# Kernel optimization log

Hardware: AMD Instinct MI355X
Metric: run time of the kernel (lower is better)

## Reference

```python
import jax, jax.numpy as jnp
import numpy as np

STATE_DIM, FAST, SLOW, ACT, HID = 256, 32, 16, 4, 256
B, T = 256, 512


def _gelu(x):
    return jax.nn.gelu(x, approximate=False)


def _gru_cell(x, h, wih, whh, bih, bhh):
    # torch GRUCell: r,z,n gates; weights are [3H, in]/[3H, H]
    gi = x @ wih.T + bih
    gh = h @ whh.T + bhh
    ir, iz, inn = jnp.split(gi, 3, axis=-1)
    hr, hz, hn = jnp.split(gh, 3, axis=-1)
    r = jax.nn.sigmoid(ir + hr)
    z = jax.nn.sigmoid(iz + hz)
    n = jnp.tanh(inn + r * hn)
    return (1.0 - z) * n + z * h


def setup_inputs() -> dict:
    key = jax.random.key(0)
    ks = jax.random.split(key, 32)
    s = 0.05
    d = {
        'states': jax.random.normal(ks[0], (B, T, STATE_DIM), jnp.float32),
        'actions': jax.random.normal(ks[1], (B, T, ACT), jnp.float32),
        'noise_fast': jax.random.normal(ks[2], (B, T, FAST), jnp.float32),
        'noise_slow': jax.random.normal(ks[3], (B, T, SLOW), jnp.float32),
        # fast encoder: Linear(256,256) GELU Linear(256,64)
        'fe_w1': jax.random.normal(ks[4], (HID, STATE_DIM)) * s,
        'fe_b1': jnp.zeros((HID,)),
        'fe_w2': jax.random.normal(ks[5], (FAST * 2, HID)) * s,
        'fe_b2': jnp.zeros((FAST * 2,)),
        # fast GRUCell(in=36, h=32)
        'fg_wih': jax.random.normal(ks[6], (3 * FAST, FAST + ACT)) * s,
        'fg_whh': jax.random.normal(ks[7], (3 * FAST, FAST)) * s,
        'fg_bih': jnp.zeros((3 * FAST,)),
        'fg_bhh': jnp.zeros((3 * FAST,)),
        # slow encoder: Linear(288,128) GELU Linear(128,32)
        'se_w1': jax.random.normal(ks[8], (HID // 2, STATE_DIM + FAST)) * s,
        'se_b1': jnp.zeros((HID // 2,)),
        'se_w2': jax.random.normal(ks[9], (SLOW * 2, HID // 2)) * s,
        'se_b2': jnp.zeros((SLOW * 2,)),
        # slow GRUCell(in=48, h=16)
        'sg_wih': jax.random.normal(ks[10], (3 * SLOW, SLOW + FAST)) * s,
        'sg_whh': jax.random.normal(ks[11], (3 * SLOW, SLOW)) * s,
        'sg_bih': jnp.zeros((3 * SLOW,)),
        'sg_bhh': jnp.zeros((3 * SLOW,)),
        # decoder: Linear(48,256) GELU Linear(256,256)
        'de_w1': jax.random.normal(ks[12], (HID, FAST + SLOW)) * s,
        'de_b1': jnp.zeros((HID,)),
        'de_w2': jax.random.normal(ks[13], (STATE_DIM, HID)) * s,
        'de_b2': jnp.zeros((STATE_DIM,)),
        'slow_update_rate': jnp.asarray(0.1, jnp.float32),
    }
    return d


def _forward(states, actions, noise_fast, noise_slow,
             fe_w1, fe_b1, fe_w2, fe_b2, fg_wih, fg_whh, fg_bih, fg_bhh,
             se_w1, se_b1, se_w2, se_b2, sg_wih, sg_whh, sg_bih, sg_bhh,
             de_w1, de_b1, de_w2, de_b2, slow_update_rate):
    Bn = states.shape[0]
    upd = jax.nn.sigmoid(slow_update_rate)

    def step(carry, xs):
        z_fast, z_slow = carry
        state, action, nf, ns = xs  # [B, ...] per-timestep slices
        # fast encoder + reparameterization
        fp = _gelu(state @ fe_w1.T + fe_b1) @ fe_w2.T + fe_b2
        f_mean, f_lv = jnp.split(fp, 2, axis=-1)
        z_fast_new = f_mean + jnp.exp(0.5 * f_lv) * nf
        z_fast = _gru_cell(jnp.concatenate([z_fast_new, action], -1), z_fast,
                           fg_wih, fg_whh, fg_bih, fg_bhh)
        # slow encoder + reparameterization
        sp = _gelu(jnp.concatenate([state, z_fast], -1) @ se_w1.T + se_b1) @ se_w2.T + se_b2
        s_mean, s_lv = jnp.split(sp, 2, axis=-1)
        z_slow_new = s_mean + jnp.exp(0.5 * s_lv) * ns
        z_slow_trans = _gru_cell(jnp.concatenate([z_slow_new, z_fast], -1), z_slow,
                                 sg_wih, sg_whh, sg_bih, sg_bhh)
        z_slow = upd * z_slow_trans + (1.0 - upd) * z_slow
        # decoder
        pred = _gelu(jnp.concatenate([z_fast, z_slow], -1) @ de_w1.T + de_b1) @ de_w2.T + de_b2
        return (z_fast, z_slow), (z_fast, z_slow, pred)

    init = (jnp.zeros((Bn, FAST), states.dtype), jnp.zeros((Bn, SLOW), states.dtype))
    xs = (states.swapaxes(0, 1), actions.swapaxes(0, 1),
          noise_fast.swapaxes(0, 1), noise_slow.swapaxes(0, 1))  # time-major [T,B,*]
    _, (zf, zs, preds) = jax.lax.scan(step, init, xs)
    return (preds.swapaxes(0, 1), zf.swapaxes(0, 1), zs.swapaxes(0, 1))


def reference(states, actions, noise_fast, noise_slow,
              fe_w1, fe_b1, fe_w2, fe_b2, fg_wih, fg_whh, fg_bih, fg_bhh,
              se_w1, se_b1, se_w2, se_b2, sg_wih, sg_whh, sg_bih, sg_bhh,
              de_w1, de_b1, de_w2, de_b2, slow_update_rate):
    # returns (predictions [B,T,state_dim], fast_latents [B,T,32], slow_latents [B,T,16])
    return _forward(states, actions, noise_fast, noise_slow,
                    fe_w1, fe_b1, fe_w2, fe_b2, fg_wih, fg_whh, fg_bih, fg_bhh,
                    se_w1, se_b1, se_w2, se_b2, sg_wih, sg_whh, sg_bih, sg_bhh,
                    de_w1, de_b1, de_w2, de_b2, slow_update_rate)
```

## Files before the change

### kernel.cpp

```cpp
#include <hip/hip_runtime.h>

typedef unsigned short u16t;
typedef __attribute__((ext_vector_type(8))) short bf16x8;
typedef __attribute__((ext_vector_type(4))) float f32x4;
typedef __attribute__((ext_vector_type(2))) float f32x2;

#define DI static __device__ __forceinline__

constexpr int Bn = 256, Tn = 512;
constexpr long Rn = (long)Bn * Tn;

DI float b2f(u16t u){ union{unsigned u32; float f;} v; v.u32 = ((unsigned)u)<<16; return v.f; }
DI u16t f2b(float f){ union{float fp; unsigned u;} v; v.fp=f; return (u16t)((v.u + 0x7fffu + ((v.u>>16)&1u))>>16); }
DI float fsigm(float x){ return __builtin_amdgcn_rcpf(1.f + __expf(-x)); }
DI float ftanh(float x){ float e = __expf(2.f*x); return 1.f - 2.f*__builtin_amdgcn_rcpf(e+1.f); }
DI float fgelu(float x){
  float t = 0.7978845608028654f*x*(1.f + 0.044715f*x*x);
  return x*(1.f - __builtin_amdgcn_rcpf(__expf(2.f*t)+1.f));
}
DI f32x4 mfma16(bf16x8 a, bf16x8 b, f32x4 c){ return __builtin_amdgcn_mfma_f32_16x16x32_bf16(a,b,c,0,0,0); }
DI unsigned pkr(float a, float b){ return (unsigned)f2b(a) | ((unsigned)f2b(b)<<16); }
DI float plo(unsigned u){ union{unsigned x; float f;} v; v.x = u<<16; return v.f; }
DI float phi(unsigned u){ union{unsigned x; float f;} v; v.x = u & 0xffff0000u; return v.f; }
DI bf16x8 mk8(unsigned w0,unsigned w1,unsigned w2,unsigned w3){
  union{unsigned u[4]; bf16x8 v;} z; z.u[0]=w0; z.u[1]=w1; z.u[2]=w2; z.u[3]=w3; return z.v;
}
DI bf16x8 ldw8(const float* p){
  f32x4 a = *(const f32x4*)p, b = *(const f32x4*)(p+4);
  return mk8(pkr(a[0],a[1]), pkr(a[2],a[3]), pkr(b[0],b[1]), pkr(b[2],b[3]));
}
DI bf16x8 zero8(){ bf16x8 v; v[0]=0;v[1]=0;v[2]=0;v[3]=0;v[4]=0;v[5]=0;v[6]=0;v[7]=0; return v; }
DI void lfence(){ asm volatile("s_waitcnt lgkmcnt(0)" ::: "memory"); __builtin_amdgcn_sched_barrier(0); }

__global__ __launch_bounds__(256) void k_pre(
    const float* __restrict__ states, const float* __restrict__ nfast,
    const float* __restrict__ fe_w1, const float* __restrict__ fe_b1,
    const float* __restrict__ fe_w2, const float* __restrict__ fe_b2,
    const float* __restrict__ se_w1, const float* __restrict__ se_b1,
    u16t* __restrict__ ws_zfn, u16t* __restrict__ ws_se1)
{
  __shared__ __align__(16) u16t s_x[64*256];
  __shared__ __align__(16) u16t s_h[64*256];
  const int tid = threadIdx.x;
  const int lane = tid & 63, wave = tid >> 6;
  const int l15 = lane & 15, lh = lane >> 4;
  const long row0 = (long)blockIdx.x * 64;

  #pragma unroll
  for (int i=0;i<8;i++){
    int c = tid + i*256;
    int row = c >> 5, col = (c & 31) << 3;
    bf16x8 v = ldw8(states + (row0+row)*256 + col);
    *(bf16x8*)&s_x[row*256 + (col ^ ((row&7)<<3))] = v;
  }
  __syncthreads();

  const int wrow = wave*16;
  const int arow = wrow + l15;
  f32x4 acc1[16], acc3[8];
  #pragma unroll
  for (int nt=0;nt<16;nt++){ float bv = fe_b1[nt*16+l15]; acc1[nt] = (f32x4){bv,bv,bv,bv}; }
  #pragma unroll
  for (int nt=0;nt<8;nt++){ float bv = se_b1[nt*16+l15]; acc3[nt] = (f32x4){bv,bv,bv,bv}; }
  #pragma unroll
  for (int kt=0;kt<8;kt++){
    int acol = kt*32 + lh*8;
    bf16x8 af = *(const bf16x8*)&s_x[arow*256 + (acol ^ ((arow&7)<<3))];
    #pragma unroll
    for (int nt=0;nt<16;nt++){
      bf16x8 bw = ldw8(fe_w1 + (nt*16+l15)*256 + acol);
      acc1[nt] = mfma16(af, bw, acc1[nt]);
    }
    #pragma unroll
    for (int nt=0;nt<8;nt++){
      bf16x8 bw = ldw8(se_w1 + (nt*16+l15)*288 + acol);
      acc3[nt] = mfma16(af, bw, acc3[nt]);
    }
  }
  #pragma unroll
  for (int nt=0;nt<8;nt++){
    #pragma unroll
    for (int r=0;r<4;r++){
      int row = wrow + lh*4 + r;
      ws_se1[(row0+row)*128 + nt*16+l15] = f2b(acc3[nt][r]);
    }
  }
  #pragma unroll
  for (int nt=0;nt<16;nt++){
    #pragma unroll
    for (int r=0;r<4;r++){
      int row = wrow + lh*4 + r; int col = nt*16 + l15;
      s_h[row*256 + (col ^ ((row&7)<<3))] = f2b(fgelu(acc1[nt][r]));
    }
  }
  __syncthreads();
  f32x4 acc2[4];
  #pragma unroll
  for (int a=0;a<4;a++){ float bv = fe_b2[a*16+l15]; acc2[a] = (f32x4){bv,bv,bv,bv}; }
  #pragma unroll
  for (int kt=0;kt<8;kt++){
    int acol = kt*32 + lh*8;
    bf16x8 af = *(const bf16x8*)&s_h[arow*256 + (acol ^ ((arow&7)<<3))];
    #pragma unroll
    for (int a=0;a<4;a++){
      bf16x8 bw = ldw8(fe_w2 + (a*16+l15)*256 + acol);
      acc2[a] = mfma16(af, bw, acc2[a]);
    }
  }
  #pragma unroll
  for (int a=0;a<2;a++){
    #pragma unroll
    for (int r=0;r<4;r++){
      int row = wrow + lh*4 + r; int col = a*16 + l15;
      float nfv = nfast[(row0+row)*32 + col];
      float zv = acc2[a][r] + __expf(0.5f*acc2[a+2][r])*nfv;
      ws_zfn[(row0+row)*32 + col] = f2b(zv);
    }
  }
}

__global__ __launch_bounds__(64,1) void k_rec(
  const u16t* __restrict__ ws_zfn, const u16t* __restrict__ ws_se1,
  const float* __restrict__ actions, const float* __restrict__ noise_slow,
  const float* __restrict__ fg_wih, const float* __restrict__ fg_whh,
  const float* __restrict__ fg_bih, const float* __restrict__ fg_bhh,
  const float* __restrict__ se_w1, const float* __restrict__ se_w2, const float* __restrict__ se_b2,
  const float* __restrict__ sg_wih, const float* __restrict__ sg_whh,
  const float* __restrict__ sg_bih, const float* __restrict__ sg_bhh,
  const float* __restrict__ updp,
  float* __restrict__ out_zf, float* __restrict__ out_zs)
{
  __shared__ __align__(16) float zfv[32], zsv[16], zfnv[32], actv[4], nsv[16];
  __shared__ __align__(16) float se1v[128], hidv[128], zsnv[16], spb[32];
  __shared__ __align__(16) float gsum[64], gni[32], gnh[32], sgib[48], sghb[48];
  const int lane = threadIdx.x;
  const int l31 = lane & 31, hf = lane >> 5;
  const long base = (long)blockIdx.x * Tn;

  unsigned wihP[18], whhP[16], wihH[9], whhH[8], wseP[2][16], wspP[32], wsgiP[24], wsghP[8];
  #pragma unroll
  for (int p=0;p<18;p++) wihP[p] = pkr(fg_wih[lane*36+2*p], fg_wih[lane*36+2*p+1]);
  #pragma unroll
  for (int p=0;p<16;p++) whhP[p] = pkr(fg_whh[lane*32+2*p], fg_whh[lane*32+2*p+1]);
  #pragma unroll
  for (int p=0;p<9;p++){ int k = hf*18+2*p;
    wihH[p] = pkr(fg_wih[(64+l31)*36 + k], fg_wih[(64+l31)*36 + k+1]); }
  #pragma unroll
  for (int p=0;p<8;p++){ int k = hf*16+2*p;
    whhH[p] = pkr(fg_whh[(64+l31)*32 + k], fg_whh[(64+l31)*32 + k+1]); }
  #pragma unroll
  for (int jj=0;jj<2;jj++){
    #pragma unroll
    for (int p=0;p<16;p++)
      wseP[jj][p] = pkr(se_w1[(lane+jj*64)*288 + 256 + 2*p], se_w1[(lane+jj*64)*288 + 256 + 2*p+1]);
  }
  #pragma unroll
  for (int p=0;p<32;p++)
    wspP[p] = pkr(se_w2[l31*128 + hf*64 + 2*p], se_w2[l31*128 + hf*64 + 2*p+1]);
  if (lane < 48){
    #pragma unroll
    for (int p=0;p<24;p++) wsgiP[p] = pkr(sg_wih[lane*48+2*p], sg_wih[lane*48+2*p+1]);
    #pragma unroll
    for (int p=0;p<8;p++)  wsghP[p] = pkr(sg_whh[lane*16+2*p], sg_whh[lane*16+2*p+1]);
  }
  const float bsum  = fg_bih[lane] + fg_bhh[lane];
  const float bni2  = fg_bih[64+l31], bnh2 = fg_bhh[64+l31];
  const float seb2L = se_b2[l31];
  const float sgbiL = sg_bih[lane<48?lane:47], sgbhL = sg_bhh[lane<48?lane:47];
  const float upd = fsigm(updp[0]);

  if (lane < 32) zfv[lane] = 0.f;
  if (lane < 16) zsv[lane] = 0.f;

  u16t pzfn = 0, ps0 = 0, ps1 = 0; float pact = 0.f, pns = 0.f;
  auto pf = [&](int tt){
    if (lane < 32) pzfn = ws_zfn[(base+tt)*32 + lane];
    ps0 = ws_se1[(base+tt)*128 + lane];
    ps1 = ws_se1[(base+tt)*128 + 64 + lane];
    if (lane < 4)  pact = actions[(base+tt)*4 + lane];
    if (lane < 16) pns  = noise_slow[(base+tt)*16 + lane];
  };
  pf(0);

  for (int t=0; t<Tn; t++){
    if (lane < 32) zfnv[lane] = b2f(pzfn);
    se1v[lane] = b2f(ps0); se1v[64+lane] = b2f(ps1);
    if (lane < 4)  actv[lane] = pact;
    if (lane < 16) nsv[lane] = pns;
    lfence();
    if (t+1 < Tn) pf(t+1);

    {
      float s = bsum;
      #pragma unroll
      for (int p=0;p<18;p++){
        f32x2 x = (p<16) ? *(const f32x2*)&zfnv[2*p] : *(const f32x2*)&actv[2*(p-16)];
        s += plo(wihP[p])*x[0] + phi(wihP[p])*x[1];
      }
      #pragma unroll
      for (int p=0;p<16;p++){
        f32x2 x = *(const f32x2*)&zfv[2*p];
        s += plo(whhP[p])*x[0] + phi(whhP[p])*x[1];
      }
      gsum[lane] = s;
      float si = 0.f, sh = 0.f;
      #pragma unroll
      for (int p=0;p<9;p++){
        int k = hf*18 + 2*p;
        f32x2 x = (k < 32) ? *(const f32x2*)&zfnv[k] : *(const f32x2*)&actv[k-32];
        si += plo(wihH[p])*x[0] + phi(wihH[p])*x[1];
      }
      #pragma unroll
      for (int p=0;p<8;p++){
        f32x2 x = *(const f32x2*)&zfv[hf*16 + 2*p];
        sh += plo(whhH[p])*x[0] + phi(whhH[p])*x[1];
      }
      si += __shfl_xor(si, 32);
      sh += __shfl_xor(sh, 32);
      if (lane < 32){ gni[lane] = si + bni2; gnh[lane] = sh + bnh2; }
    }
    lfence();
    if (lane < 32){
      float r = fsigm(gsum[lane]);
      float z = fsigm(gsum[32+lane]);
      float n = ftanh(gni[lane] + r*gnh[lane]);
      float h2 = (1.f-z)*n + z*zfv[lane];
      zfv[lane] = h2;
      out_zf[(base+t)*32 + lane] = h2;
    }
    lfence();
    #pragma unroll
    for (int jj=0;jj<2;jj++){
      float s = se1v[lane + jj*64];
      #pragma unroll
      for (int p=0;p<16;p++){
        f32x2 x = *(const f32x2*)&zfv[2*p];
        s += plo(wseP[jj][p])*x[0] + phi(wseP[jj][p])*x[1];
      }
      hidv[lane + jj*64] = fgelu(s);
    }
    lfence();
    {
      float s = 0.f;
      #pragma unroll
      for (int p=0;p<32;p++){
        f32x2 x = *(const f32x2*)&hidv[hf*64 + 2*p];
        s += plo(wspP[p])*x[0] + phi(wspP[p])*x[1];
      }
      s += __shfl_xor(s, 32);
      if (lane < 32) spb[lane] = s + seb2L;
    }
    lfence();
    if (lane < 16) zsnv[lane] = spb[lane] + __expf(0.5f*spb[16+lane])*nsv[lane];
    lfence();
    if (lane < 48){
      float gi = sgbiL, gh = sgbhL;
      #pragma unroll
      for (int p=0;p<24;p++){
        f32x2 x = (p<8) ? *(const f32x2*)&zsnv[2*p] : *(const f32x2*)&zfv[2*p-16];
        gi += plo(wsgiP[p])*x[0] + phi(wsgiP[p])*x[1];
      }
      #pragma unroll
      for (int p=0;p<8;p++){
        f32x2 x = *(const f32x2*)&zsv[2*p];
        gh += plo(wsghP[p])*x[0] + phi(wsghP[p])*x[1];
      }
      sgib[lane] = gi; sghb[lane] = gh;
    }
    lfence();
    if (lane < 16){
      float r = fsigm(sgib[lane] + sghb[lane]);
      float z = fsigm(sgib[16+lane] + sghb[16+lane]);
      float n = ftanh(sgib[32+lane] + r*sghb[32+lane]);
      float zt = (1.f-z)*n + z*zsv[lane];
      float zn = upd*zt + (1.f-upd)*zsv[lane];
      zsv[lane] = zn;
      out_zs[(base+t)*16 + lane] = zn;
    }
    lfence();
  }
}

__global__ __launch_bounds__(256) void k_dec(
  const float* __restrict__ izf, const float* __restrict__ izs,
  const float* __restrict__ de_w1, const float* __restrict__ de_b1,
  const float* __restrict__ de_w2, const float* __restrict__ de_b2,
  float* __restrict__ preds)
{
  __shared__ __align__(16) u16t s_a[64*64];
  __shared__ __align__(16) u16t s_h[64*256];
  const int tid = threadIdx.x;
  const int lane = tid & 63, wave = tid >> 6;
  const int l15 = lane & 15, lh = lane >> 4;
  const long row0 = (long)blockIdx.x * 64;

  { int row = tid >> 2, col = (tid & 3) << 3;
    bf16x8 v = ldw8(izf + (row0+row)*32 + col);
    *(bf16x8*)&s_a[row*64 + (col ^ ((row&7)<<3))] = v; }
  if (tid < 128){
    int row = tid >> 1, col = 32 + ((tid & 1) << 3);
    bf16x8 v = ldw8(izs + (row0+row)*16 + ((tid&1)<<3));
    *(bf16x8*)&s_a[row*64 + (col ^ ((row&7)<<3))] = v;
  } else {
    int t2 = tid - 128;
    int row = t2 >> 1, col = 48 + ((t2 & 1) << 3);
    bf16x8 v = zero8();
    *(bf16x8*)&s_a[row*64 + (col ^ ((row&7)<<3))] = v;
  }
  __syncthreads();

  const int wrow = wave*16;
  const int arow = wrow + l15;
  f32x4 acc[16];
  #pragma unroll
  for (int nt=0;nt<16;nt++){ float bv = de_b1[nt*16+l15]; acc[nt] = (f32x4){bv,bv,bv,bv}; }
  #pragma unroll
  for (int kt=0;kt<2;kt++){
    int acol = kt*32 + lh*8;
    bf16x8 af = *(const bf16x8*)&s_a[arow*64 + (acol ^ ((arow&7)<<3))];
    #pragma unroll
    for (int nt=0;nt<16;nt++){
      bf16x8 bw = zero8();
      if (!(kt==1 && lh>=2)) bw = ldw8(de_w1 + (nt*16+l15)*48 + acol);
      acc[nt] = mfma16(af, bw, acc[nt]);
    }
  }
  #pragma unroll
  for (int nt=0;nt<16;nt++){
    #pragma unroll
    for (int r=0;r<4;r++){
      int row = wrow + lh*4 + r; int col = nt*16 + l15;
      s_h[row*256 + (col ^ ((row&7)<<3))] = f2b(fgelu(acc[nt][r]));
    }
  }
  __syncthreads();
  f32x4 a2[16];
  #pragma unroll
  for (int nt=0;nt<16;nt++){ float bv = de_b2[nt*16+l15]; a2[nt] = (f32x4){bv,bv,bv,bv}; }
  #pragma unroll
  for (int kt=0;kt<8;kt++){
    int acol = kt*32 + lh*8;
    bf16x8 af = *(const bf16x8*)&s_h[arow*256 + (acol ^ ((arow&7)<<3))];
    #pragma unroll
    for (int nt=0;nt<16;nt++){
      bf16x8 bw = ldw8(de_w2 + (nt*16+l15)*256 + acol);
      a2[nt] = mfma16(af, bw, a2[nt]);
    }
  }
  #pragma unroll
  for (int nt=0;nt<16;nt++){
    #pragma unroll
    for (int r=0;r<4;r++){
      int row = wrow + lh*4 + r;
      preds[(row0+row)*256 + nt*16+l15] = a2[nt][r];
    }
  }
}

extern "C" void kernel_launch(void* const* d_in, const int* in_sizes, int n_in,
                              void* d_out, int out_size, void* d_ws, size_t ws_size,
                              hipStream_t stream)
{
  if (n_in < 25 || in_sizes[0] != (int)(Rn*256) || in_sizes[8] != 96*36 ||
      in_sizes[12] != 128*288 || in_sizes[20] != 256*48 || in_sizes[24] != 1)
    return;
  if (out_size != (int)(Rn*304))
    return;

  const float* states = (const float*)d_in[0];
  const float* actions= (const float*)d_in[1];
  const float* nfast  = (const float*)d_in[2];
  const float* nslow  = (const float*)d_in[3];
  const float* fe_w1  = (const float*)d_in[4];
  const float* fe_b1  = (const float*)d_in[5];
  const float* fe_w2  = (const float*)d_in[6];
  const float* fe_b2  = (const float*)d_in[7];
  const float* fg_wih = (const float*)d_in[8];
  const float* fg_whh = (const float*)d_in[9];
  const float* fg_bih = (const float*)d_in[10];
  const float* fg_bhh = (const float*)d_in[11];
  const float* se_w1  = (const float*)d_in[12];
  const float* se_b1  = (const float*)d_in[13];
  const float* se_w2  = (const float*)d_in[14];
  const float* se_b2  = (const float*)d_in[15];
  const float* sg_wih = (const float*)d_in[16];
  const float* sg_whh = (const float*)d_in[17];
  const float* sg_bih = (const float*)d_in[18];
  const float* sg_bhh = (const float*)d_in[19];
  const float* de_w1  = (const float*)d_in[20];
  const float* de_b1  = (const float*)d_in[21];
  const float* de_w2  = (const float*)d_in[22];
  const float* de_b2  = (const float*)d_in[23];
  const float* updp   = (const float*)d_in[24];

  float* preds = (float*)d_out;
  float* ozf = preds + Rn*256;
  float* ozs = ozf + Rn*32;

  size_t need = (size_t)Rn*320;
  u16t* ws_zfn; u16t* ws_se1;
  if (ws_size >= need){
    ws_zfn = (u16t*)d_ws;
    ws_se1 = ws_zfn + Rn*32;
  } else {
    ws_zfn = (u16t*)preds;
    ws_se1 = ws_zfn + Rn*32;
  }

  k_pre<<<(int)(Rn/64), 256, 0, stream>>>(states, nfast,
      fe_w1, fe_b1, fe_w2, fe_b2, se_w1, se_b1, ws_zfn, ws_se1);
  k_rec<<<Bn, 64, 0, stream>>>(ws_zfn, ws_se1, actions, nslow,
      fg_wih, fg_whh, fg_bih, fg_bhh, se_w1, se_w2, se_b2,
      sg_wih, sg_whh, sg_bih, sg_bhh, updp, ozf, ozs);
  k_dec<<<(int)(Rn/64), 256, 0, stream>>>(ozf, ozs, de_w1, de_b1, de_w2, de_b2, preds);
}
```

Baseline: 2.134 ms.

## Interleave two batch rows per wave in the recurrence and replace LDS round-trips with shuffles

The recurrent kernel now has each 64-lane block advance two independent batch sequences together. The aim is to hide the latency of each serial step with independent work, and the grid shrinks to half as many blocks. Several LDS writes and fences for gate partial sums are replaced by cross-lane shuffles and register-held state, which cuts synchronisation per timestep. Weights are kept as fp32 registers instead of packed bf16, and the bf16 packing in ldw8 uses the hardware v_cvt_pk_bf16_f32 instruction. The larger register footprint risks spilling, and only half as many CUs are used.

```diff
diff --git a/kernel.cpp b/kernel.cpp
--- a/kernel.cpp
+++ b/kernel.cpp
@@ -19,15 +19,17 @@
   return x*(1.f - __builtin_amdgcn_rcpf(__expf(2.f*t)+1.f));
 }
 DI f32x4 mfma16(bf16x8 a, bf16x8 b, f32x4 c){ return __builtin_amdgcn_mfma_f32_16x16x32_bf16(a,b,c,0,0,0); }
-DI unsigned pkr(float a, float b){ return (unsigned)f2b(a) | ((unsigned)f2b(b)<<16); }
-DI float plo(unsigned u){ union{unsigned x; float f;} v; v.x = u<<16; return v.f; }
-DI float phi(unsigned u){ union{unsigned x; float f;} v; v.x = u & 0xffff0000u; return v.f; }
+DI unsigned cvtpk(float a, float b){
+  unsigned r;
+  asm("v_cvt_pk_bf16_f32 %0, %1, %2" : "=v"(r) : "v"(a), "v"(b));
+  return r;
+}
 DI bf16x8 mk8(unsigned w0,unsigned w1,unsigned w2,unsigned w3){
   union{unsigned u[4]; bf16x8 v;} z; z.u[0]=w0; z.u[1]=w1; z.u[2]=w2; z.u[3]=w3; return z.v;
 }
 DI bf16x8 ldw8(const float* p){
   f32x4 a = *(const f32x4*)p, b = *(const f32x4*)(p+4);
-  return mk8(pkr(a[0],a[1]), pkr(a[2],a[3]), pkr(b[0],b[1]), pkr(b[2],b[3]));
+  return mk8(cvtpk(a[0],a[1]), cvtpk(a[2],a[3]), cvtpk(b[0],b[1]), cvtpk(b[2],b[3]));
 }
 DI bf16x8 zero8(){ bf16x8 v; v[0]=0;v[1]=0;v[2]=0;v[3]=0;v[4]=0;v[5]=0;v[6]=0;v[7]=0; return v; }
 DI void lfence(){ asm volatile("s_waitcnt lgkmcnt(0)" ::: "memory"); __builtin_amdgcn_sched_barrier(0); }
@@ -130,38 +132,35 @@
   const float* __restrict__ updp,
   float* __restrict__ out_zf, float* __restrict__ out_zs)
 {
-  __shared__ __align__(16) float zfv[32], zsv[16], zfnv[32], actv[4], nsv[16];
-  __shared__ __align__(16) float se1v[128], hidv[128], zsnv[16], spb[32];
-  __shared__ __align__(16) float gsum[64], gni[32], gnh[32], sgib[48], sghb[48];
+  __shared__ __align__(16) float zfnv[2][32], actv[2][4];
+  __shared__ __align__(16) float zfv[2][32], zsv[2][16], zsnv[2][16];
+  __shared__ __align__(16) float hidv[2][128];
   const int lane = threadIdx.x;
   const int l31 = lane & 31, hf = lane >> 5;
-  const long base = (long)blockIdx.x * Tn;
-
-  unsigned wihP[18], whhP[16], wihH[9], whhH[8], wseP[2][16], wspP[32], wsgiP[24], wsghP[8];
-  #pragma unroll
-  for (int p=0;p<18;p++) wihP[p] = pkr(fg_wih[lane*36+2*p], fg_wih[lane*36+2*p+1]);
-  #pragma unroll
-  for (int p=0;p<16;p++) whhP[p] = pkr(fg_whh[lane*32+2*p], fg_whh[lane*32+2*p+1]);
-  #pragma unroll
-  for (int p=0;p<9;p++){ int k = hf*18+2*p;
-    wihH[p] = pkr(fg_wih[(64+l31)*36 + k], fg_wih[(64+l31)*36 + k+1]); }
-  #pragma unroll
-  for (int p=0;p<8;p++){ int k = hf*16+2*p;
-    whhH[p] = pkr(fg_whh[(64+l31)*32 + k], fg_whh[(64+l31)*32 + k+1]); }
+  const long base0 = (long)(2*blockIdx.x    ) * Tn;
+  const long base1 = (long)(2*blockIdx.x + 1) * Tn;
+
+  float wih[36], whh[32], wihH[18], whhH[16], wse[2][32], wsp[64], wsgi[48], wsgh[16];
+  #pragma unroll
+  for (int k=0;k<36;k++) wih[k] = fg_wih[lane*36+k];
+  #pragma unroll
+  for (int k=0;k<32;k++) whh[k] = fg_whh[lane*32+k];
+  #pragma unroll
+  for (int j=0;j<18;j++) wihH[j] = fg_wih[(64+l31)*36 + hf*18 + j];
+  #pragma unroll
+  for (int j=0;j<16;j++) whhH[j] = fg_whh[(64+l31)*32 + hf*16 + j];
   #pragma unroll
   for (int jj=0;jj<2;jj++){
     #pragma unroll
-    for (int p=0;p<16;p++)
-      wseP[jj][p] = pkr(se_w1[(lane+jj*64)*288 + 256 + 2*p], se_w1[(lane+jj*64)*288 + 256 + 2*p+1]);
-  }
-  #pragma unroll
-  for (int p=0;p<32;p++)
-    wspP[p] = pkr(se_w2[l31*128 + hf*64 + 2*p], se_w2[l31*128 + hf*64 + 2*p+1]);
+    for (int k=0;k<32;k++) wse[jj][k] = se_w1[(lane+jj*64)*288 + 256 + k];
+  }
+  #pragma unroll
+  for (int k=0;k<64;k++) wsp[k] = se_w2[l31*128 + hf*64 + k];
   if (lane < 48){
     #pragma unroll
-    for (int p=0;p<24;p++) wsgiP[p] = pkr(sg_wih[lane*48+2*p], sg_wih[lane*48+2*p+1]);
-    #pragma unroll
-    for (int p=0;p<8;p++)  wsghP[p] = pkr(sg_whh[lane*16+2*p], sg_whh[lane*16+2*p+1]);
+    for (int k=0;k<48;k++) wsgi[k] = sg_wih[lane*48+k];
+    #pragma unroll
+    for (int k=0;k<16;k++) wsgh[k] = sg_whh[lane*16+k];
   }
   const float bsum  = fg_bih[lane] + fg_bhh[lane];
   const float bni2  = fg_bih[64+l31], bnh2 = fg_bhh[64+l31];
@@ -169,115 +168,136 @@
   const float sgbiL = sg_bih[lane<48?lane:47], sgbhL = sg_bhh[lane<48?lane:47];
   const float upd = fsigm(updp[0]);
 
-  if (lane < 32) zfv[lane] = 0.f;
-  if (lane < 16) zsv[lane] = 0.f;
-
-  u16t pzfn = 0, ps0 = 0, ps1 = 0; float pact = 0.f, pns = 0.f;
+  if (lane < 32){ zfv[0][lane]=0.f; zfv[1][lane]=0.f; }
+  if (lane < 16){ zsv[0][lane]=0.f; zsv[1][lane]=0.f; }
+  float zf_r[2] = {0.f,0.f};
+  float zs_r[2] = {0.f,0.f};
+
+  u16t pzfn[2], ps0[2], ps1[2]; float pact[2], pns[2];
   auto pf = [&](int tt){
-    if (lane < 32) pzfn = ws_zfn[(base+tt)*32 + lane];
-    ps0 = ws_se1[(base+tt)*128 + lane];
-    ps1 = ws_se1[(base+tt)*128 + 64 + lane];
-    if (lane < 4)  pact = actions[(base+tt)*4 + lane];
-    if (lane < 16) pns  = noise_slow[(base+tt)*16 + lane];
+    if (lane < 32){ pzfn[0]=ws_zfn[(base0+tt)*32+lane]; pzfn[1]=ws_zfn[(base1+tt)*32+lane]; }
+    ps0[0]=ws_se1[(base0+tt)*128+lane];    ps0[1]=ws_se1[(base1+tt)*128+lane];
+    ps1[0]=ws_se1[(base0+tt)*128+64+lane]; ps1[1]=ws_se1[(base1+tt)*128+64+lane];
+    if (lane < 4){ pact[0]=actions[(base0+tt)*4+lane]; pact[1]=actions[(base1+tt)*4+lane]; }
+    if (lane < 16){ pns[0]=noise_slow[(base0+tt)*16+lane]; pns[1]=noise_slow[(base1+tt)*16+lane]; }
   };
   pf(0);
 
   for (int t=0; t<Tn; t++){
-    if (lane < 32) zfnv[lane] = b2f(pzfn);
-    se1v[lane] = b2f(ps0); se1v[64+lane] = b2f(ps1);
-    if (lane < 4)  actv[lane] = pact;
-    if (lane < 16) nsv[lane] = pns;
+    float se1a[2], se1c[2], nsq[2];
+    #pragma unroll
+    for (int q=0;q<2;q++){
+      if (lane < 32) zfnv[q][lane] = b2f(pzfn[q]);
+      if (lane < 4)  actv[q][lane] = pact[q];
+      se1a[q] = b2f(ps0[q]); se1c[q] = b2f(ps1[q]); nsq[q] = pns[q];
+    }
     lfence();
     if (t+1 < Tn) pf(t+1);
 
-    {
+    #pragma unroll
+    for (int q=0;q<2;q++){
       float s = bsum;
       #pragma unroll
-      for (int p=0;p<18;p++){
-        f32x2 x = (p<16) ? *(const f32x2*)&zfnv[2*p] : *(const f32x2*)&actv[2*(p-16)];
-        s += plo(wihP[p])*x[0] + phi(wihP[p])*x[1];
-      }
-      #pragma unroll
-      for (int p=0;p<16;p++){
-        f32x2 x = *(const f32x2*)&zfv[2*p];
-        s += plo(whhP[p])*x[0] + phi(whhP[p])*x[1];
-      }
-      gsum[lane] = s;
+      for (int p=0;p<8;p++){
+        f32x4 x = *(const f32x4*)&zfnv[q][4*p];
+        s += wih[4*p]*x[0] + wih[4*p+1]*x[1] + wih[4*p+2]*x[2] + wih[4*p+3]*x[3];
+      }
+      { f32x4 x = *(const f32x4*)&actv[q][0];
+        s += wih[32]*x[0] + wih[33]*x[1] + wih[34]*x[2] + wih[35]*x[3]; }
+      #pragma unroll
+      for (int p=0;p<8;p++){
+        f32x4 x = *(const f32x4*)&zfv[q][4*p];
+        s += whh[4*p]*x[0] + whh[4*p+1]*x[1] + whh[4*p+2]*x[2] + whh[4*p+3]*x[3];
+      }
       float si = 0.f, sh = 0.f;
       #pragma unroll
-      for (int p=0;p<9;p++){
-        int k = hf*18 + 2*p;
-        f32x2 x = (k < 32) ? *(const f32x2*)&zfnv[k] : *(const f32x2*)&actv[k-32];
-        si += plo(wihH[p])*x[0] + phi(wihH[p])*x[1];
-      }
-      #pragma unroll
-      for (int p=0;p<8;p++){
-        f32x2 x = *(const f32x2*)&zfv[hf*16 + 2*p];
-        sh += plo(whhH[p])*x[0] + phi(whhH[p])*x[1];
+      for (int j=0;j<9;j++){
+        int k = hf*18 + 2*j;
+        const float* xp = (k < 32) ? &zfnv[q][k] : &actv[q][k-32];
+        f32x2 xx = *(const f32x2*)xp;
+        si += wihH[2*j]*xx[0] + wihH[2*j+1]*xx[1];
+      }
+      #pragma unroll
+      for (int j=0;j<8;j++){
+        f32x2 xx = *(const f32x2*)&zfv[q][hf*16 + 2*j];
+        sh += whhH[2*j]*xx[0] + whhH[2*j+1]*xx[1];
       }
       si += __shfl_xor(si, 32);
       sh += __shfl_xor(sh, 32);
-      if (lane < 32){ gni[lane] = si + bni2; gnh[lane] = sh + bnh2; }
+      float sz = __shfl_xor(s, 32);
+      if (lane < 32){
+        float r = fsigm(s);
+        float z = fsigm(sz);
+        float n = ftanh((si + bni2) + r*(sh + bnh2));
+        float h2 = (1.f-z)*n + z*zf_r[q];
+        zf_r[q] = h2;
+        zfv[q][lane] = h2;
+        out_zf[((q?base1:base0)+t)*32 + lane] = h2;
+      }
     }
     lfence();
-    if (lane < 32){
-      float r = fsigm(gsum[lane]);
-      float z = fsigm(gsum[32+lane]);
-      float n = ftanh(gni[lane] + r*gnh[lane]);
-      float h2 = (1.f-z)*n + z*zfv[lane];
-      zfv[lane] = h2;
-      out_zf[(base+t)*32 + lane] = h2;
+    #pragma unroll
+    for (int q=0;q<2;q++){
+      #pragma unroll
+      for (int jj=0;jj<2;jj++){
+        float s = jj ? se1c[q] : se1a[q];
+        #pragma unroll
+        for (int p=0;p<8;p++){
+          f32x4 x = *(const f32x4*)&zfv[q][4*p];
+          s += wse[jj][4*p]*x[0] + wse[jj][4*p+1]*x[1] + wse[jj][4*p+2]*x[2] + wse[jj][4*p+3]*x[3];
+        }
+        hidv[q][lane + jj*64] = fgelu(s);
+      }
     }
     lfence();
     #pragma unroll
-    for (int jj=0;jj<2;jj++){
-      float s = se1v[lane + jj*64];
+    for (int q=0;q<2;q++){
+      float s = 0.f;
       #pragma unroll
       for (int p=0;p<16;p++){
-        f32x2 x = *(const f32x2*)&zfv[2*p];
-        s += plo(wseP[jj][p])*x[0] + phi(wseP[jj][p])*x[1];
-      }
-      hidv[lane + jj*64] = fgelu(s);
+        f32x4 x = *(const f32x4*)&hidv[q][hf*64 + 4*p];
+        s += wsp[4*p]*x[0] + wsp[4*p+1]*x[1] + wsp[4*p+2]*x[2] + wsp[4*p+3]*x[3];
+      }
+      s += __shfl_xor(s, 32);
+      float spo = s + seb2L;
+      float sphi = __shfl(spo, (lane+16)&63);
+      if (lane < 16){
+        float zn = spo + __expf(0.5f*sphi)*nsq[q];
+        zsnv[q][lane] = zn;
+      }
     }
     lfence();
-    {
-      float s = 0.f;
-      #pragma unroll
-      for (int p=0;p<32;p++){
-        f32x2 x = *(const f32x2*)&hidv[hf*64 + 2*p];
-        s += plo(wspP[p])*x[0] + phi(wspP[p])*x[1];
-      }
-      s += __shfl_xor(s, 32);
-      if (lane < 32) spb[lane] = s + seb2L;
-    }
-    lfence();
-    if (lane < 16) zsnv[lane] = spb[lane] + __expf(0.5f*spb[16+lane])*nsv[lane];
-    lfence();
-    if (lane < 48){
+    #pragma unroll
+    for (int q=0;q<2;q++){
       float gi = sgbiL, gh = sgbhL;
       #pragma unroll
-      for (int p=0;p<24;p++){
-        f32x2 x = (p<8) ? *(const f32x2*)&zsnv[2*p] : *(const f32x2*)&zfv[2*p-16];
-        gi += plo(wsgiP[p])*x[0] + phi(wsgiP[p])*x[1];
+      for (int p=0;p<4;p++){
+        f32x4 x = *(const f32x4*)&zsnv[q][4*p];
+        gi += wsgi[4*p]*x[0] + wsgi[4*p+1]*x[1] + wsgi[4*p+2]*x[2] + wsgi[4*p+3]*x[3];
       }
       #pragma unroll
       for (int p=0;p<8;p++){
-        f32x2 x = *(const f32x2*)&zsv[2*p];
-        gh += plo(wsghP[p])*x[0] + phi(wsghP[p])*x[1];
-      }
-      sgib[lane] = gi; sghb[lane] = gh;
-    }
-    lfence();
-    if (lane < 16){
-      float r = fsigm(sgib[lane] + sghb[lane]);
-      float z = fsigm(sgib[16+lane] + sghb[16+lane]);
-      float n = ftanh(sgib[32+lane] + r*sghb[32+lane]);
-      float zt = (1.f-z)*n + z*zsv[lane];
-      float zn = upd*zt + (1.f-upd)*zsv[lane];
-      zsv[lane] = zn;
-      out_zs[(base+t)*16 + lane] = zn;
-    }
-    lfence();
+        f32x4 x = *(const f32x4*)&zfv[q][4*p];
+        gi += wsgi[16+4*p]*x[0] + wsgi[16+4*p+1]*x[1] + wsgi[16+4*p+2]*x[2] + wsgi[16+4*p+3]*x[3];
+      }
+      #pragma unroll
+      for (int p=0;p<4;p++){
+        f32x4 x = *(const f32x4*)&zsv[q][4*p];
+        gh += wsgh[4*p]*x[0] + wsgh[4*p+1]*x[1] + wsgh[4*p+2]*x[2] + wsgh[4*p+3]*x[3];
+      }
+      float gi_z = __shfl(gi, (lane+16)&63), gi_n = __shfl(gi, (lane+32)&63);
+      float gh_z = __shfl(gh, (lane+16)&63), gh_n = __shfl(gh, (lane+32)&63);
+      if (lane < 16){
+        float r = fsigm(gi + gh);
+        float z = fsigm(gi_z + gh_z);
+        float n = ftanh(gi_n + r*gh_n);
+        float zt = (1.f-z)*n + z*zs_r[q];
+        float zn = upd*zt + (1.f-upd)*zs_r[q];
+        zs_r[q] = zn;
+        zsv[q][lane] = zn;
+        out_zs[((q?base1:base0)+t)*16 + lane] = zn;
+      }
+    }
   }
 }
 
@@ -409,7 +429,7 @@
 
   k_pre<<<(int)(Rn/64), 256, 0, stream>>>(states, nfast,
       fe_w1, fe_b1, fe_w2, fe_b2, se_w1, se_b1, ws_zfn, ws_se1);
-  k_rec<<<Bn, 64, 0, stream>>>(ws_zfn, ws_se1, actions, nslow,
+  k_rec<<<Bn/2, 64, 0, stream>>>(ws_zfn, ws_se1, actions, nslow,
       fg_wih, fg_whh, fg_bih, fg_bhh, se_w1, se_w2, se_b2,
       sg_wih, sg_whh, sg_bih, sg_bhh, updp, ozf, ozs);
   k_dec<<<(int)(Rn/64), 256, 0, stream>>>(ozf, ozs, de_w1, de_b1, de_w2, de_b2, preds);
```

New measurement: 3.204 ms. +50.1%, slower.
